# Kernel optimization log

Measured on AMD Instinct MI355X. Metric: run time of the kernel, lower is better.

## Reference

```python
import jax, jax.numpy as jnp
import numpy as np

N, P, M, NCLS = 32, 24564, 32, 81
NEG_POS_RATIO, ALPHA, THRESHOLD = 3, 1.0, 0.5
BACKGROUND = NCLS  # sentinel label for background priors (== n_classes, as in original)


def _rand_boxes(key, prefix):
    # valid normalized xyxy boxes (x2>x1, y2>y1, inside [0,1])
    k1, k2 = jax.random.split(key)
    cxy = jax.random.uniform(k1, prefix + (2,), minval=0.1, maxval=0.9)
    wh = jax.random.uniform(k2, prefix + (2,), minval=0.02, maxval=0.2)
    return jnp.concatenate([cxy - wh / 2, cxy + wh / 2], axis=-1)


def setup_inputs() -> dict:
    key = jax.random.key(0)
    ks = jax.random.split(key, 6)
    return {
        "predicted_boxes": jax.random.normal(ks[0], (N, P, 4), jnp.float32),
        "predicted_class_dist": jax.random.normal(ks[1], (N, P, NCLS), jnp.float32),
        "predicted_objectness": jax.random.uniform(ks[2], (N, P), jnp.float32),
        "anchor_priors": _rand_boxes(ks[3], (P,)),
        "boxes": _rand_boxes(ks[4], (N, M)),
        "labels": jax.random.randint(ks[5], (N, M), 0, NCLS),
    }


def xy_to_cxcy(xy):
    return jnp.concatenate([(xy[..., :2] + xy[..., 2:]) / 2, xy[..., 2:] - xy[..., :2]], axis=-1)


def cxcy_to_gcxgcy(cxcy, priors_cxcy):
    return jnp.concatenate([
        (cxcy[..., :2] - priors_cxcy[..., :2]) / (priors_cxcy[..., 2:] / 10.0),
        jnp.log(cxcy[..., 2:] / priors_cxcy[..., 2:]) * 5.0,
    ], axis=-1)


def box_iou(a, b):  # a: (M,4), b: (P,4) -> (M,P)
    lt = jnp.maximum(a[:, None, :2], b[None, :, :2])
    rb = jnp.minimum(a[:, None, 2:], b[None, :, 2:])
    wh = jnp.clip(rb - lt, 0.0)
    inter = wh[..., 0] * wh[..., 1]
    area_a = (a[:, 2] - a[:, 0]) * (a[:, 3] - a[:, 1])
    area_b = (b[:, 2] - b[:, 0]) * (b[:, 3] - b[:, 1])
    return inter / (area_a[:, None] + area_b[None, :] - inter)


def _match(boxes_i, labels_i, priors):
    # per-image anchor matching (vmapped over batch)
    iou = box_iou(boxes_i, priors)                     # (M, P)
    iou_per_prior = iou.max(axis=0)                    # (P,)
    obj_per_prior = iou.argmax(axis=0)                 # (P,)
    prior_per_obj = iou.argmax(axis=1)                 # (M,)
    obj_per_prior = obj_per_prior.at[prior_per_obj].set(jnp.arange(M))
    iou_per_prior = iou_per_prior.at[prior_per_obj].set(1.0)
    label_per_prior = labels_i[obj_per_prior]
    label_per_prior = jnp.where(iou_per_prior < THRESHOLD, BACKGROUND, label_per_prior)
    true_locs = cxcy_to_gcxgcy(xy_to_cxcy(boxes_i[obj_per_prior]), xy_to_cxcy(priors))
    return true_locs, label_per_prior


def reference(predicted_boxes, predicted_class_dist, predicted_objectness, anchor_priors, boxes, labels):
    true_locs, true_classes = jax.vmap(_match, in_axes=(0, 0, None))(boxes, labels, anchor_priors)
    pos = true_classes != BACKGROUND                   # (N, P) bool
    n_pos_total = pos.sum().astype(jnp.float32)
    posf = pos.astype(jnp.float32)

    # smooth L1 over positive priors (mean over selected elements)
    diff = predicted_boxes - true_locs
    ad = jnp.abs(diff)
    sl1 = jnp.where(ad < 1.0, 0.5 * diff * diff, ad - 0.5)
    loc_loss = jnp.sum(sl1 * posf[..., None]) / (n_pos_total * 4.0)

    # cross entropy over positive priors (mean)
    logp = jax.nn.log_softmax(predicted_class_dist, axis=-1)
    safe_cls = jnp.where(pos, true_classes, 0)
    ce = -jnp.take_along_axis(logp, safe_cls[..., None], axis=-1)[..., 0]
    class_loss_pos = jnp.sum(ce * posf) / n_pos_total

    # objectness MSE: positive mean + hard-negative mining
    obj_loss = (predicted_objectness - posf) ** 2      # (N, P)
    obj_loss_pos = jnp.sum(obj_loss * posf) / n_pos_total

    neg_loss = jnp.where(pos, 0.0, obj_loss)
    neg_sorted = -jnp.sort(-neg_loss, axis=1)          # descending per row
    n_hard = NEG_POS_RATIO * pos.sum(axis=1)           # (N,)
    hmask = (jnp.arange(P)[None, :] < n_hard[:, None]).astype(jnp.float32)
    obj_loss_hardneg = jnp.sum(neg_sorted * hmask) / jnp.maximum(hmask.sum(), 1.0)

    return class_loss_pos + obj_loss_pos + obj_loss_hardneg + ALPHA * loc_loss
```

## Files before the change

### kernel.cpp

```cpp
#include <hip/hip_runtime.h>
#include <math.h>

#define NB 32
#define PP 24564
#define MM 32
#define NCLS 81
#define CHUNK 1024
#define MBLK 24
#define PPW 768
#define BSH 18
#define HB 4096
#define CAPL 2048

#define WS_DONE   0
#define WS_PCNT   32
#define WS_IACC   160
#define WS_PACC   672
#define WS_CPART  9888
#define WS_BKEYP  12960
#define WS_POSBIT 209568
#define WS_M8     307872
#define WS_VAL    1093936

__device__ __forceinline__ float sl1(float d) {
    float a = fabsf(d);
    return a < 1.0f ? 0.5f * d * d : a - 0.5f;
}
__device__ __forceinline__ unsigned long long u64max(unsigned long long a, unsigned long long b) {
    return a > b ? a : b;
}
__device__ __forceinline__ float locv(const float4& pd, const float4& pb,
                                      float gx1, float gy1, float gx2, float gy2) {
    float pcx = (pb.x + pb.z) * 0.5f, pcy = (pb.y + pb.w) * 0.5f;
    float pw = pb.z - pb.x, ph = pb.w - pb.y;
    float g0 = ((gx1 + gx2) * 0.5f - pcx) / (pw / 10.0f);
    float g1 = ((gy1 + gy2) * 0.5f - pcy) / (ph / 10.0f);
    float g2 = logf((gx2 - gx1) / pw) * 5.0f;
    float g3 = logf((gy2 - gy1) / ph) * 5.0f;
    return sl1(pd.x - g0) + sl1(pd.y - g1) + sl1(pd.z - g2) + sl1(pd.w - g3);
}

extern "C" __global__ void __launch_bounds__(256) k_match(
    const float* __restrict__ priors,
    const float* __restrict__ boxes,
    const float* __restrict__ obj,
    const float* __restrict__ pred_boxes,
    const float* __restrict__ pred_cls,
    const int* __restrict__ labels,
    unsigned long long* __restrict__ bkeyp,
    unsigned int* __restrict__ posbit,
    unsigned char* __restrict__ m8,
    float* __restrict__ val,
    int* __restrict__ cpart,
    float* __restrict__ pacc,
    int* __restrict__ done)
{
    const int n = blockIdx.y;
    const int t = threadIdx.x;
    const int lane = t & 63;
    const int wave = t >> 6;
    const int bx = blockIdx.x;
    const int p0 = bx * CHUNK;

    if (bx == 0 && n == 0 && t == 0) *done = 0;

    __shared__ unsigned char sm8[CHUNK];
    __shared__ float bx0[MM], by0[MM], bx1[MM], by1[MM], bar_[MM];
    __shared__ unsigned long long wk[4][MM];
    __shared__ int bcnt;
    __shared__ float sacc[3];

    float4 pr0, pr1, pr2, pr3;
    float ov[4];
    {
        const float4 dummy = make_float4(3.f, 3.f, 3.5f, 3.5f);
        int p;
        p = p0 + t;        if (p < PP) { pr0 = *(const float4*)(priors + (size_t)p * 4); ov[0] = obj[(size_t)n * PP + p]; } else { pr0 = dummy; ov[0] = 0.f; }
        p = p0 + t + 256;  if (p < PP) { pr1 = *(const float4*)(priors + (size_t)p * 4); ov[1] = obj[(size_t)n * PP + p]; } else { pr1 = dummy; ov[1] = 0.f; }
        p = p0 + t + 512;  if (p < PP) { pr2 = *(const float4*)(priors + (size_t)p * 4); ov[2] = obj[(size_t)n * PP + p]; } else { pr2 = dummy; ov[2] = 0.f; }
        p = p0 + t + 768;  if (p < PP) { pr3 = *(const float4*)(priors + (size_t)p * 4); ov[3] = obj[(size_t)n * PP + p]; } else { pr3 = dummy; ov[3] = 0.f; }
    }
    if (t < MM) {
        const float* b = boxes + ((size_t)n * MM + t) * 4;
        float x1 = b[0], y1 = b[1], x2 = b[2], y2 = b[3];
        bx0[t] = x1; by0[t] = y1; bx1[t] = x2; by1[t] = y2;
        bar_[t] = (x2 - x1) * (y2 - y1);
    }
    if (t == 0) bcnt = 0;
    if (t < 3) sacc[t] = 0.f;
    __syncthreads();

    const float pa0 = (pr0.z - pr0.x) * (pr0.w - pr0.y);
    const float pa1 = (pr1.z - pr1.x) * (pr1.w - pr1.y);
    const float pa2 = (pr2.z - pr2.x) * (pr2.w - pr2.y);
    const float pa3 = (pr3.z - pr3.x) * (pr3.w - pr3.y);
    unsigned pb0 = 0, pb1 = 0, pb2 = 0, pb3 = 0;

#define DO_IOU(PR, PA, PB, ROFF) { \
        float w = fminf(x1, PR.z) - fmaxf(x0, PR.x); \
        float h = fminf(y1, PR.w) - fmaxf(y0, PR.y); \
        w = fmaxf(w, 0.0f); h = fmaxf(h, 0.0f); \
        float inter = w * h; \
        float iou = inter * __builtin_amdgcn_rcpf(ar + PA - inter); \
        unsigned ib = __float_as_uint(iou); \
        unsigned nk = (ib & 0xFFFFFFE0u) | (unsigned)(31 - m); \
        PB = PB > nk ? PB : nk; \
        unsigned long long kk = ((unsigned long long)ib << 32) \
            | (unsigned long long)(0xFFFFFFFFu - (unsigned)(p0 + t + (ROFF))); \
        km = u64max(km, kk); }

#pragma unroll 2
    for (int m = 0; m < MM; m++) {
        const float x0 = bx0[m], y0 = by0[m], x1 = bx1[m], y1 = by1[m], ar = bar_[m];
        unsigned long long km = 0ULL;
        DO_IOU(pr0, pa0, pb0, 0)
        DO_IOU(pr1, pa1, pb1, 256)
        DO_IOU(pr2, pa2, pb2, 512)
        DO_IOU(pr3, pa3, pb3, 768)
#pragma unroll
        for (int d = 1; d < 64; d <<= 1)
            km = u64max(km, (unsigned long long)__shfl_xor(km, d));
        if (lane == 0) wk[wave][m] = km;
    }
#undef DO_IOU

    int cnt = 0;
    unsigned long long bl[4];
#define ROWOUT(PB, R) { \
        int p = p0 + t + (R) * 256; \
        bool pos = (PB >= 0x3F000000u) && (p < PP); \
        unsigned long long ball = __ballot(pos); \
        bl[R] = ball; \
        unsigned char mb = (unsigned char)(31u - (PB & 31u)); \
        sm8[t + (R) * 256] = mb; \
        if (lane == 0) { \
            int wi = n * PPW + ((p0 + (R) * 256 + wave * 64) >> 5); \
            posbit[wi] = (unsigned)ball; posbit[wi + 1] = (unsigned)(ball >> 32); \
            cnt += __popcll(ball); \
        } \
        if (p < PP) { \
            size_t idx = (size_t)n * PP + p; \
            m8[idx] = mb; \
            val[idx] = pos ? 0.f : ov[R] * ov[R]; \
        } }
    ROWOUT(pb0, 0) ROWOUT(pb1, 1) ROWOUT(pb2, 2) ROWOUT(pb3, 3)
#undef ROWOUT
    if (lane == 0 && cnt) atomicAdd(&bcnt, cnt);

    {
        const int half = lane >> 5, hl = lane & 31;
        float ce_s = 0.f, loc_s = 0.f, op_s = 0.f;
#pragma unroll
        for (int R = 0; R < 4; R++) {
            unsigned long long mask = bl[R];
            const int roff = R * 256 + wave * 64;
            while (mask) {
                int i1 = __ffsll((long long)mask) - 1; mask &= mask - 1;
                int i2 = -1;
                if (mask) { i2 = __ffsll((long long)mask) - 1; mask &= mask - 1; }
                const int pi = half ? i2 : i1;
                const bool act = pi >= 0;
                const int poff = roff + (act ? pi : 0);
                const size_t idx = (size_t)n * PP + p0 + poff;

                const int bm = sm8[poff];
                const float* row = pred_cls + idx * NCLS;
                float a = act ? row[hl] : -INFINITY;
                float b = act ? row[hl + 32] : -INFINITY;
                float c = (act && hl < NCLS - 64) ? row[hl + 64] : -INFINITY;
                float mx = fmaxf(fmaxf(a, b), c);
#pragma unroll
                for (int d = 1; d < 32; d <<= 1) mx = fmaxf(mx, __shfl_xor(mx, d));
                float se = act ? (expf(a - mx) + expf(b - mx)
                                  + ((hl < NCLS - 64) ? expf(c - mx) : 0.f)) : 0.f;
#pragma unroll
                for (int d = 1; d < 32; d <<= 1) se += __shfl_xor(se, d);

                if (act) {
                    if (hl == 0) {
                        ce_s += mx + logf(se) - row[labels[n * MM + bm]];
                    } else if (hl == 1) {
                        float4 pb = *(const float4*)(priors + (size_t)(p0 + poff) * 4);
                        float4 pd = *(const float4*)(pred_boxes + idx * 4);
                        loc_s += locv(pd, pb, bx0[bm], by0[bm], bx1[bm], by1[bm]);
                    } else if (hl == 2) {
                        float o = obj[idx];
                        op_s += (o - 1.0f) * (o - 1.0f);
                    }
                }
            }
        }
        if (ce_s != 0.f)  atomicAdd(&sacc[0], ce_s);
        if (loc_s != 0.f) atomicAdd(&sacc[1], loc_s);
        if (op_s != 0.f)  atomicAdd(&sacc[2], op_s);
    }

    __syncthreads();
    if (t == 0) {
        cpart[n * MBLK + bx] = bcnt;
        float* pa = pacc + ((size_t)n * MBLK + bx) * 3;
        pa[0] = sacc[0]; pa[1] = sacc[1]; pa[2] = sacc[2];
    }
    if (t < MM) {
        unsigned long long r = u64max(u64max(wk[0][t], wk[1][t]),
                                      u64max(wk[2][t], wk[3][t]));
        bkeyp[((size_t)n * MBLK + bx) * MM + t] = r;
    }
}

extern "C" __global__ void __launch_bounds__(512) k_fin(
    const float* __restrict__ priors,
    const float* __restrict__ boxes,
    const float* __restrict__ obj,
    const float* __restrict__ pred_boxes,
    const float* __restrict__ pred_cls,
    const int* __restrict__ labels,
    const unsigned long long* __restrict__ bkeyp,
    const unsigned int* __restrict__ posbit,
    const unsigned char* __restrict__ m8,
    const int* __restrict__ cpart,
    const float* __restrict__ pacc,
    float* __restrict__ val,
    int* __restrict__ pcnt,
    float4* __restrict__ iacc,
    int* __restrict__ done,
    float* __restrict__ out)
{
    const int n = blockIdx.x;
    const int t = threadIdx.x;
    const int lane = t & 63;
    const int wave = t >> 6;
    float* v = val + (size_t)n * PP;
    const float4* v4 = (const float4*)v;
    const int N4 = PP / 4;

    __shared__ unsigned fl[MM];
    __shared__ int newlist[MM];
    __shared__ int s_nnew, s_nat, s_tot;
    __shared__ float sacc[3];
    __shared__ float wred[8], wred2[8];

    if (t < 3) sacc[t] = 0.f;
    if (t == 0) { s_nnew = 0; s_nat = 0; }
    __syncthreads();

    if (t < MM) {
        const unsigned long long* bp = bkeyp + (size_t)n * MBLK * MM + t;
        unsigned long long r = 0ULL;
#pragma unroll
        for (int s = 0; s < MBLK; s++) r = u64max(r, bp[(size_t)s * MM]);
        fl[t] = ~(unsigned)(r & 0xFFFFFFFFULL);
    }
    if (t < MBLK) atomicAdd(&s_nat, cpart[n * MBLK + t]);
    __syncthreads();

    float d_ce = 0.f, d_loc = 0.f;
    if (t < MM) {
        unsigned p = fl[t];
        bool owner = true;
        for (int j = t + 1; j < MM; j++) if (fl[j] == p) owner = false;
        if (owner) {
            size_t idx = (size_t)n * PP + p;
            bool natPos = (posbit[n * PPW + (p >> 5)] >> (p & 31)) & 1u;
            if (natPos) {
                int bmn = (int)m8[idx];
                if (bmn != t) {
                    const float* row = pred_cls + idx * NCLS;
                    d_ce = row[labels[n * MM + bmn]] - row[labels[n * MM + t]];
                    float4 pb = *(const float4*)(priors + (size_t)p * 4);
                    float4 pd = *(const float4*)(pred_boxes + idx * 4);
                    const float* bf = boxes + ((size_t)n * MM + t) * 4;
                    const float* bn = boxes + ((size_t)n * MM + bmn) * 4;
                    d_loc = locv(pd, pb, bf[0], bf[1], bf[2], bf[3])
                          - locv(pd, pb, bn[0], bn[1], bn[2], bn[3]);
                }
            } else {
                int ix = atomicAdd(&s_nnew, 1);
                newlist[ix] = ((int)p << 5) | t;
                v[p] = 0.f;
            }
        }
    }
    if (t < 64) {
#pragma unroll
        for (int d = 1; d < 64; d <<= 1) {
            d_ce += __shfl_xor(d_ce, d);
            d_loc += __shfl_xor(d_loc, d);
        }
        if (t == 0) {
            if (d_ce != 0.f)  atomicAdd(&sacc[0], d_ce);
            if (d_loc != 0.f) atomicAdd(&sacc[1], d_loc);
        }
    }
    if (t < MBLK * 3) atomicAdd(&sacc[t % 3], pacc[(size_t)n * MBLK * 3 + t]);
    __syncthreads();

    const int nn = s_nnew;
    {
        const int hl = lane & 31;
        float nce = 0.f, nloc = 0.f, nop = 0.f;
        for (int i = wave; i < nn; i += 8) {
            int e = newlist[i];
            int p = e >> 5, bm = e & 31;
            size_t idx = (size_t)n * PP + p;
            const float* row = pred_cls + idx * NCLS;
            bool al = lane < 32;
            float a = al ? row[hl] : -INFINITY;
            float b = al ? row[hl + 32] : -INFINITY;
            float c = (al && hl < NCLS - 64) ? row[hl + 64] : -INFINITY;
            float mx = fmaxf(fmaxf(a, b), c);
#pragma unroll
            for (int d = 1; d < 32; d <<= 1) mx = fmaxf(mx, __shfl_xor(mx, d));
            float se = al ? (expf(a - mx) + expf(b - mx)
                             + ((hl < NCLS - 64) ? expf(c - mx) : 0.f)) : 0.f;
#pragma unroll
            for (int d = 1; d < 32; d <<= 1) se += __shfl_xor(se, d);
            if (lane == 0) {
                nce += mx + logf(se) - row[labels[n * MM + bm]];
            } else if (lane == 1) {
                float4 pb = *(const float4*)(priors + (size_t)p * 4);
                float4 pd = *(const float4*)(pred_boxes + idx * 4);
                const float* bb = boxes + ((size_t)n * MM + bm) * 4;
                nloc += locv(pd, pb, bb[0], bb[1], bb[2], bb[3]);
            } else if (lane == 2) {
                float o = obj[idx];
                nop += (o - 1.0f) * (o - 1.0f);
            }
        }
        if (nce != 0.f)  atomicAdd(&sacc[0], nce);
        if (nloc != 0.f) atomicAdd(&sacc[1], nloc);
        if (nop != 0.f)  atomicAdd(&sacc[2], nop);
    }
    __syncthreads();
    if (t == 0) s_tot = s_nat + s_nnew;
    __syncthreads();
    const int s_tot_v = s_tot;
    int k = s_tot_v * 3; if (k > PP) k = PP;

    float result = 0.f;
    if (k >= PP) {
        float s = 0.f;
        for (int i = t; i < N4; i += 512) {
            float4 q = v4[i]; s += q.x + q.y + q.z + q.w;
        }
#pragma unroll
        for (int d = 32; d > 0; d >>= 1) s += __shfl_down(s, d);
        if ((t & 63) == 0) wred[wave] = s;
        __syncthreads();
        if (t == 0) { for (int i = 0; i < 8; i++) result += wred[i]; }
    } else if (k > 0) {
        __shared__ unsigned hist[HB];
        __shared__ unsigned ssc[512];
        __shared__ unsigned cand[CAPL];
        __shared__ int s_c, s_d, s_rem;
        __shared__ unsigned s_cur;
        __shared__ int s_rr;
        __shared__ unsigned rh[128];

        for (int i = t; i < HB; i += 512) hist[i] = 0;
        if (t == 0) s_c = 0;
        __syncthreads();

        for (int i = t; i < N4; i += 512) {
            float4 q = v4[i];
            atomicAdd(&hist[__float_as_uint(q.x) >> BSH], 1u);
            atomicAdd(&hist[__float_as_uint(q.y) >> BSH], 1u);
            atomicAdd(&hist[__float_as_uint(q.z) >> BSH], 1u);
            atomicAdd(&hist[__float_as_uint(q.w) >> BSH], 1u);
        }
        __syncthreads();

        unsigned csum = 0;
#pragma unroll
        for (int j = 0; j < 8; j++) csum += hist[4095 - 8 * t - j];
        ssc[t] = csum; __syncthreads();
        for (int off = 1; off < 512; off <<= 1) {
            unsigned x = (t >= off) ? ssc[t - off] : 0u;
            __syncthreads(); ssc[t] += x; __syncthreads();
        }
        unsigned incl = ssc[t], excl = incl - csum;
        if (excl < (unsigned)k && incl >= (unsigned)k) {
            unsigned cum = excl;
#pragma unroll
            for (int j = 0; j < 8; j++) {
                int b = 4095 - 8 * t - j; unsigned h = hist[b];
                if (cum + h >= (unsigned)k) { s_d = b; s_rem = (int)((unsigned)k - cum); break; }
                cum += h;
            }
        }
        __syncthreads();
        const int d = s_d; const int rem0 = s_rem;

        float ms = 0.f;
        for (int i = t; i < N4; i += 512) {
            float4 q = v4[i];
#define HND(C) { unsigned b = __float_as_uint(C); int bn = (int)(b >> BSH); \
            if (bn > d) ms += (C); \
            else if (bn == d) { int ix = atomicAdd(&s_c, 1); if (ix < CAPL) cand[ix] = b; } }
            HND(q.x) HND(q.y) HND(q.z) HND(q.w)
#undef HND
        }
        __syncthreads();
        const int C = s_c;
        const bool okl = (C <= CAPL);

        unsigned cur = (unsigned)d << BSH; int rem = rem0;
        const int shs[3] = {11, 4, 0};
        const int wbs[3] = {7, 7, 4};
        for (int ps = 0; ps < 3; ps++) {
            const int sh = shs[ps], wb = wbs[ps], W = 1 << wb;
            if (t < W) rh[t] = 0;
            __syncthreads();
            if (okl) {
                for (int i = t; i < C; i += 512) {
                    unsigned b = cand[i];
                    if ((b >> (sh + wb)) == (cur >> (sh + wb)))
                        atomicAdd(&rh[(b >> sh) & (W - 1)], 1u);
                }
            } else {
                for (int i = t; i < PP; i += 512) {
                    unsigned b = __float_as_uint(v[i]);
                    if ((b >> (sh + wb)) == (cur >> (sh + wb)))
                        atomicAdd(&rh[(b >> sh) & (W - 1)], 1u);
                }
            }
            __syncthreads();
            if (t == 0) {
                unsigned cum = 0; int dd;
                for (dd = W - 1; dd > 0; --dd) {
                    unsigned h = rh[dd];
                    if (cum + h >= (unsigned)rem) break;
                    cum += h;
                }
                s_cur = cur | ((unsigned)dd << sh);
                s_rr = rem - (int)cum;
            }
            __syncthreads();
            cur = s_cur; rem = s_rr;
            __syncthreads();
        }
        const unsigned thr = cur;
        const float thrv = __uint_as_float(thr);

        float sg = ms, cg = 0.f;
        if (okl) {
            for (int i = t; i < C; i += 512) {
                unsigned b = cand[i];
                if (b > thr) { sg += __uint_as_float(b); cg += 1.f; }
            }
        } else {
            for (int i = t; i < PP; i += 512) {
                unsigned b = __float_as_uint(v[i]);
                if ((int)(b >> BSH) == d && b > thr) { sg += __uint_as_float(b); cg += 1.f; }
            }
        }
#pragma unroll
        for (int dd = 32; dd > 0; dd >>= 1) {
            sg += __shfl_down(sg, dd);
            cg += __shfl_down(cg, dd);
        }
        if ((t & 63) == 0) { wred[wave] = sg; wred2[wave] = cg; }
        __syncthreads();
        if (t == 0) {
            float S = 0.f, Cc = 0.f;
            for (int i = 0; i < 8; i++) { S += wred[i]; Cc += wred2[i]; }
            result = S + ((float)rem0 - Cc) * thrv;
        }
    }

    if (t == 0) {
        pcnt[n] = s_tot_v;
        iacc[n] = make_float4(sacc[0], sacc[1], sacc[2], result);
        __threadfence();
        int old = atomicAdd(done, 1);
        if (old == NB - 1) {
            __threadfence();
            int np = 0, den = 0; float ce = 0.f, lc = 0.f, op = 0.f, hs = 0.f;
            for (int i = 0; i < NB; i++) {
                int c = pcnt[i];
                np += c;
                int kk = c * 3; if (kk > PP) kk = PP;
                den += kk;
                float4 a = iacc[i];
                ce += a.x; lc += a.y; op += a.z; hs += a.w;
            }
            float npf = (float)np;
            out[0] = ce / npf + op / npf
                   + hs / fmaxf((float)den, 1.0f)
                   + lc / (npf * 4.0f);
        }
    }
}

extern "C" void kernel_launch(void* const* d_in, const int* in_sizes, int n_in,
                              void* d_out, int out_size, void* d_ws, size_t ws_size,
                              hipStream_t stream) {
    const float* pred_boxes = (const float*)d_in[0];
    const float* pred_cls   = (const float*)d_in[1];
    const float* pred_obj   = (const float*)d_in[2];
    const float* priors     = (const float*)d_in[3];
    const float* boxes      = (const float*)d_in[4];
    const int*   labels     = (const int*)d_in[5];

    char* ws = (char*)d_ws;
    int* done  = (int*)(ws + WS_DONE);
    int* pcnt  = (int*)(ws + WS_PCNT);
    float4* iacc = (float4*)(ws + WS_IACC);
    float* pacc = (float*)(ws + WS_PACC);
    int* cpart = (int*)(ws + WS_CPART);
    unsigned long long* bkeyp = (unsigned long long*)(ws + WS_BKEYP);
    unsigned* posbit = (unsigned*)(ws + WS_POSBIT);
    unsigned char* m8 = (unsigned char*)(ws + WS_M8);
    float* val = (float*)(ws + WS_VAL);

    k_match<<<dim3(MBLK, NB), 256, 0, stream>>>(priors, boxes, pred_obj, pred_boxes,
                                                pred_cls, labels, bkeyp, posbit, m8,
                                                val, cpart, pacc, done);
    k_fin<<<NB, 512, 0, stream>>>(priors, boxes, pred_obj, pred_boxes, pred_cls,
                                  labels, bkeyp, posbit, m8, cpart, pacc, val,
                                  pcnt, iacc, done, (float*)d_out);
}
```

Baseline: 78.63 us.

## Batch per-object wave max reductions with butterfly fold across 32 objects

Replaces the per-object 6-step wave shuffle reduction (32 objects × 6 shuffles of u64) with a transposed fold that halves the live array each step, so each lane ends up owning one object's maximum, using about 31 shuffles instead of 192. The per-prior best IoU tracking changes from packed integer keys to an explicit float compare plus index, and the object loop is fully unrolled. It costs 32 live u64 registers per thread, which may raise VGPR pressure and lower occupancy. The tie-breaking for per-prior argmax also shifts slightly (first max rather than packed low-bit ordering).

```diff
diff --git a/kernel.cpp b/kernel.cpp
--- a/kernel.cpp
+++ b/kernel.cpp
@@ -94,45 +94,59 @@
     const float pa1 = (pr1.z - pr1.x) * (pr1.w - pr1.y);
     const float pa2 = (pr2.z - pr2.x) * (pr2.w - pr2.y);
     const float pa3 = (pr3.z - pr3.x) * (pr3.w - pr3.y);
-    unsigned pb0 = 0, pb1 = 0, pb2 = 0, pb3 = 0;
-
-#define DO_IOU(PR, PA, PB, ROFF) { \
+
+    float bst0 = -1.f, bst1 = -1.f, bst2 = -1.f, bst3 = -1.f;
+    int bm0 = 0, bm1 = 0, bm2 = 0, bm3 = 0;
+    const unsigned ip0 = 0xFFFFFFFFu - (unsigned)(p0 + t);
+    const unsigned ip1 = ip0 - 256;
+    const unsigned ip2 = ip0 - 512;
+    const unsigned ip3 = ip0 - 768;
+
+    unsigned long long cur[MM];
+
+#define DO_IOU(PR, PA, BST, BM, IP) { \
         float w = fminf(x1, PR.z) - fmaxf(x0, PR.x); \
         float h = fminf(y1, PR.w) - fmaxf(y0, PR.y); \
         w = fmaxf(w, 0.0f); h = fmaxf(h, 0.0f); \
         float inter = w * h; \
         float iou = inter * __builtin_amdgcn_rcpf(ar + PA - inter); \
-        unsigned ib = __float_as_uint(iou); \
-        unsigned nk = (ib & 0xFFFFFFE0u) | (unsigned)(31 - m); \
-        PB = PB > nk ? PB : nk; \
-        unsigned long long kk = ((unsigned long long)ib << 32) \
-            | (unsigned long long)(0xFFFFFFFFu - (unsigned)(p0 + t + (ROFF))); \
+        if (iou > BST) { BST = iou; BM = m; } \
+        unsigned long long kk = ((unsigned long long)__float_as_uint(iou) << 32) \
+                              | (unsigned long long)(IP); \
         km = u64max(km, kk); }
 
-#pragma unroll 2
+#pragma unroll
     for (int m = 0; m < MM; m++) {
         const float x0 = bx0[m], y0 = by0[m], x1 = bx1[m], y1 = by1[m], ar = bar_[m];
         unsigned long long km = 0ULL;
-        DO_IOU(pr0, pa0, pb0, 0)
-        DO_IOU(pr1, pa1, pb1, 256)
-        DO_IOU(pr2, pa2, pb2, 512)
-        DO_IOU(pr3, pa3, pb3, 768)
-#pragma unroll
-        for (int d = 1; d < 64; d <<= 1)
-            km = u64max(km, (unsigned long long)__shfl_xor(km, d));
-        if (lane == 0) wk[wave][m] = km;
+        DO_IOU(pr0, pa0, bst0, bm0, ip0)
+        DO_IOU(pr1, pa1, bst1, bm1, ip1)
+        DO_IOU(pr2, pa2, bst2, bm2, ip2)
+        DO_IOU(pr3, pa3, bst3, bm3, ip3)
+        cur[m] = km;
     }
 #undef DO_IOU
+
+#define FOLD(X, L2) { const bool hi = (lane & (X)) != 0; \
+        _Pragma("unroll") \
+        for (int j = 0; j < (L2); j++) { \
+            unsigned long long give = hi ? cur[j] : cur[j + (L2)]; \
+            unsigned long long got = __shfl_xor(give, (X)); \
+            unsigned long long keep = hi ? cur[j + (L2)] : cur[j]; \
+            cur[j] = u64max(keep, got); } }
+    FOLD(32, 16) FOLD(16, 8) FOLD(8, 4) FOLD(4, 2) FOLD(2, 1)
+#undef FOLD
+    cur[0] = u64max(cur[0], (unsigned long long)__shfl_xor(cur[0], 1));
+    if (!(lane & 1)) wk[wave][(lane >> 1) & 31] = cur[0];
 
     int cnt = 0;
     unsigned long long bl[4];
-#define ROWOUT(PB, R) { \
+#define ROWOUT(BST, BM, R) { \
         int p = p0 + t + (R) * 256; \
-        bool pos = (PB >= 0x3F000000u) && (p < PP); \
+        bool pos = (BST >= 0.5f) && (p < PP); \
         unsigned long long ball = __ballot(pos); \
         bl[R] = ball; \
-        unsigned char mb = (unsigned char)(31u - (PB & 31u)); \
-        sm8[t + (R) * 256] = mb; \
+        sm8[t + (R) * 256] = (unsigned char)(BM); \
         if (lane == 0) { \
             int wi = n * PPW + ((p0 + (R) * 256 + wave * 64) >> 5); \
             posbit[wi] = (unsigned)ball; posbit[wi + 1] = (unsigned)(ball >> 32); \
@@ -140,10 +154,10 @@
         } \
         if (p < PP) { \
             size_t idx = (size_t)n * PP + p; \
-            m8[idx] = mb; \
+            m8[idx] = (unsigned char)(BM); \
             val[idx] = pos ? 0.f : ov[R] * ov[R]; \
         } }
-    ROWOUT(pb0, 0) ROWOUT(pb1, 1) ROWOUT(pb2, 2) ROWOUT(pb3, 3)
+    ROWOUT(bst0, bm0, 0) ROWOUT(bst1, bm1, 1) ROWOUT(bst2, bm2, 2) ROWOUT(bst3, bm3, 3)
 #undef ROWOUT
     if (lane == 0 && cnt) atomicAdd(&bcnt, cnt);
 
```

Result: slower. 105.9 us (+34.7%).
